# Performance work log

Hardware: AMD Instinct MI355X
Metric: run time of the kernel (lower is better)

The kernel has to match this reference:

```python
import jax, jax.numpy as jnp
import numpy as np


def setup_inputs() -> dict:
    key = jax.random.key(0)
    kx, kw = jax.random.split(key)
    A_MAX = 16  # activations in [0, 2**A_bits - 1] = [0, 15]
    W_MAX = 15  # torch.randint(0, 2**W_bits - 1) -> [0, 14]
    x = jax.random.randint(kx, (32, 256, 56, 56), 0, A_MAX, dtype=jnp.int32)
    weight = jax.random.randint(kw, (256, 256, 3, 3), 0, W_MAX, dtype=jnp.int32)
    return {"x": x, "weight": weight}


def reference(x, weight):
    # Low-bit quantized conv2d: direct_conv2d(x.int(), w.int(), stride=1) with the
    # module's crop for (k=3, padding=1) is equivalent to a conv with padding=1.
    # Max accumulator value = 15*14*9*256 < 2**24, so fp32 accumulation is exact.
    xf = x.astype(jnp.float32)
    wf = weight.astype(jnp.float32)
    y = jax.lax.conv_general_dilated(
        xf, wf,
        window_strides=(1, 1),
        padding=((1, 1), (1, 1)),
        dimension_numbers=("NCHW", "OIHW", "NCHW"),
    )
    return y.astype(jnp.int32)  # [32, 256, 56, 56]
```

## Files before the change

### kernel.cpp

```cpp
#include <hip/hip_runtime.h>

typedef int v4i  __attribute__((ext_vector_type(4)));
typedef int v16i __attribute__((ext_vector_type(16)));

#define N_IMG   32
#define C_IN    256
#define HWDIM   56
#define HW2     3136
#define OUT_TOT 25690112
#define OUT_NSTR 802816

#define PXB     272
#define PPI     3364
#define XP_IMG  915008
#define XP_SLACK 4096
#define WP_CB2STR 73728
#define WP_BYTES  589824ull

#define S_TILE  64
#define TILES_PER_IMG 49
#define WIN_B   50048

__global__ void dc_x_to_nhwc(const int* __restrict__ x, unsigned int* __restrict__ x8,
                             int n0) {
    __shared__ unsigned int lds[64 * 65];
    const int t = threadIdx.x;
    const int w = t & 63, q = t >> 6;
    const int nl = blockIdx.x / HWDIM, h = blockIdx.x % HWDIM;

    if (w < HWDIM) {
        const int* xb = x + (size_t)(n0 + nl) * OUT_NSTR + h * HWDIM + w;
        #pragma unroll
        for (int it = 0; it < 16; ++it) {
            const int cg4 = q * 16 + it;
            const int ci0 = cg4 * 4;
            unsigned v  =  ((unsigned)xb[(ci0 + 0) * HW2] & 0xff);
            v |= ((unsigned)xb[(ci0 + 1) * HW2] & 0xff) << 8;
            v |= ((unsigned)xb[(ci0 + 2) * HW2] & 0xff) << 16;
            v |= ((unsigned)xb[(ci0 + 3) * HW2] & 0xff) << 24;
            lds[w * 65 + cg4] = v;
        }
    }
    __syncthreads();
    unsigned int* ob = x8 + (size_t)nl * (PPI * (PXB / 4)) + ((h + 1) * 58 + 1) * (PXB / 4);
    #pragma unroll
    for (int it = 0; it < 14; ++it) {
        const int f = it * 256 + t;
        const int w2 = f >> 6, cg = f & 63;
        if (w2 < HWDIM) ob[w2 * (PXB / 4) + cg] = lds[w2 * 65 + cg];
    }
}

__global__ void dc_halo(unsigned int* __restrict__ x8) {
    const int nl = blockIdx.x;
    const int t = threadIdx.x;
    if (t < 228) {
        int h, w;
        if (t < 58)       { h = 0;        w = t; }
        else if (t < 116) { h = 57;       w = t - 58; }
        else if (t < 172) { h = t - 115;  w = 0; }
        else              { h = t - 171;  w = 57; }
        unsigned int* p = x8 + ((size_t)nl * PPI + h * 58 + w) * (PXB / 4);
        #pragma unroll
        for (int i = 0; i < PXB / 4; ++i) p[i] = 0;
    }
}

__global__ void dc_pack_w(const int* __restrict__ wt, unsigned int* __restrict__ wp) {
    const int tid = blockIdx.x * 256 + threadIdx.x;
    const int jq = tid & 3;
    const int l  = (tid >> 2) & 63;
    const int kb = (tid >> 8) & 7;
    const int r  = tid >> 11;
    const int t  = r % 9;
    const int cb2 = r / 9;
    const int co  = cb2 * 32 + (l & 31);
    const int ci0 = kb * 32 + (l >> 5) * 16 + jq * 4;
    const int kh = t / 3, kw = t - kh * 3;
    unsigned v = 0;
    #pragma unroll
    for (int k = 0; k < 4; ++k) {
        unsigned b = (unsigned)wt[((co * C_IN + ci0 + k) * 3 + kh) * 3 + kw];
        v |= (b & 0xff) << (8 * k);
    }
    wp[tid] = v;
}

__device__ __forceinline__ void gll16(const char* g, char* l) {
    __builtin_amdgcn_global_load_lds(
        (const __attribute__((address_space(1))) unsigned int*)g,
        (__attribute__((address_space(3))) unsigned int*)l, 16, 0, 0);
}

__global__ __launch_bounds__(256, 3) void dc_mfma(const char* __restrict__ x8,
                                                  const char* __restrict__ wp,
                                                  int* __restrict__ out, int nwg) {
    extern __shared__ __align__(16) char xs[];

    const int bid = blockIdx.x;
    const int q = nwg >> 3, r = nwg & 7;
    const int xcd = bid & 7, bidx = bid >> 3;
    const int wgid = (xcd < r ? xcd * (q + 1) : r * (q + 1) + (xcd - r) * q) + bidx;

    const int nl = wgid / TILES_PER_IMG, st = wgid - nl * TILES_PER_IMG;

    const int tid = threadIdx.x;
    const int l = tid & 63, wid = tid >> 6;
    const int lane31 = l & 31, hi = l >> 5;

    const int hw0 = st * S_TILE;
    const int h0 = hw0 / HWDIM, w0 = hw0 - h0 * HWDIM;
    const int p0 = h0 * 58 + w0;
    const char* gsrc = x8 + (size_t)nl * XP_IMG + (size_t)p0 * PXB;

    #pragma unroll
    for (int c = 0; c < 13; ++c) {
        const int off = (c * 256 + tid) * 16;
        if (off < WIN_B) gll16(gsrc + off, xs + off);
    }

    int breg[2], outb[2];
    #pragma unroll
    for (int ni = 0; ni < 2; ++ni) {
        const int hw = hw0 + ni * 32 + lane31;
        const int h = hw / HWDIM, w = hw - h * HWDIM;
        const int p = (h + 1) * 58 + (w + 1);
        breg[ni] = (p - p0) * PXB + hi * 16 - 16048;
        outb[ni] = nl * OUT_NSTR + hw;
    }

    const char* wb0 = wp + (wid * 2) * WP_CB2STR + l * 16;
    const char* wb1 = wb0 + WP_CB2STR;

    const int xoffp[9] = {
        16048 - 59 * PXB, 16048 - 58 * PXB, 16048 - 57 * PXB,
        16048 - 1 * PXB,  16048,            16048 + 1 * PXB,
        16048 + 57 * PXB, 16048 + 58 * PXB, 16048 + 59 * PXB
    };

    __syncthreads();

    v16i acc[2][2] = {};
    v4i wa[4][2];
    v4i xb[2][2];

    wa[0][0] = *(const v4i*)(wb0);
    wa[0][1] = *(const v4i*)(wb1);
    wa[1][0] = *(const v4i*)(wb0 + 1024);
    wa[1][1] = *(const v4i*)(wb1 + 1024);
    wa[2][0] = *(const v4i*)(wb0 + 2048);
    wa[2][1] = *(const v4i*)(wb1 + 2048);
    xb[0][0] = *(const v4i*)(xs + breg[0] + xoffp[0]);
    xb[0][1] = *(const v4i*)(xs + breg[1] + xoffp[0]);

    #pragma unroll
    for (int j = 0; j < 72; ++j) {
        const int jc = j & 3;
        const int pc = j & 1;
        if (j + 3 < 72) {
            const int jn = (j + 3) & 3;
            wa[jn][0] = *(const v4i*)(wb0 + (j + 3) * 1024);
            wa[jn][1] = *(const v4i*)(wb1 + (j + 3) * 1024);
        }
        if (j + 1 < 72) {
            const int t1 = (j + 1) >> 3, kb1 = (j + 1) & 7;
            const int xo = xoffp[t1] + kb1 * 32;
            xb[pc ^ 1][0] = *(const v4i*)(xs + breg[0] + xo);
            xb[pc ^ 1][1] = *(const v4i*)(xs + breg[1] + xo);
        }
        __builtin_amdgcn_s_setprio(1);
        acc[0][0] = __builtin_amdgcn_mfma_i32_32x32x32_i8(wa[jc][0], xb[pc][0], acc[0][0], 0, 0, 0);
        acc[0][1] = __builtin_amdgcn_mfma_i32_32x32x32_i8(wa[jc][0], xb[pc][1], acc[0][1], 0, 0, 0);
        acc[1][0] = __builtin_amdgcn_mfma_i32_32x32x32_i8(wa[jc][1], xb[pc][0], acc[1][0], 0, 0, 0);
        acc[1][1] = __builtin_amdgcn_mfma_i32_32x32x32_i8(wa[jc][1], xb[pc][1], acc[1][1], 0, 0, 0);
        __builtin_amdgcn_s_setprio(0);
    }

    #pragma unroll
    for (int mi = 0; mi < 2; ++mi) {
        #pragma unroll
        for (int ni = 0; ni < 2; ++ni) {
            const v16i c = acc[mi][ni];
            int* ob = out + outb[ni] + (wid * 64 + mi * 32 + 4 * hi) * HW2;
            #pragma unroll
            for (int rr = 0; rr < 16; ++rr) {
                __builtin_nontemporal_store(c[rr], ob + ((rr & 3) + 8 * (rr >> 2)) * HW2);
            }
        }
    }
}

__global__ void dc_naive(const int* __restrict__ x, const int* __restrict__ wt,
                         int* __restrict__ out) {
    const int idx = blockIdx.x * 256 + threadIdx.x;
    if (idx >= OUT_TOT) return;
    const int w = idx % HWDIM;
    const int h = (idx / HWDIM) % HWDIM;
    const int co = (idx / HW2) & 255;
    const int n = idx / OUT_NSTR;
    const int* xn = x + n * OUT_NSTR;
    const int* wo = wt + co * (C_IN * 9);
    int acc = 0;
    for (int ci = 0; ci < C_IN; ++ci) {
        const int* xc = xn + ci * HW2;
        const int* wc = wo + ci * 9;
        #pragma unroll
        for (int kh = 0; kh < 3; ++kh) {
            const int hh = h + kh - 1;
            if ((unsigned)hh >= HWDIM) continue;
            #pragma unroll
            for (int kw = 0; kw < 3; ++kw) {
                const int ww = w + kw - 1;
                if ((unsigned)ww >= HWDIM) continue;
                acc += xc[hh * HWDIM + ww] * wc[kh * 3 + kw];
            }
        }
    }
    out[idx] = acc;
}

extern "C" void kernel_launch(void* const* d_in, const int* in_sizes, int n_in,
                              void* d_out, int out_size, void* d_ws, size_t ws_size,
                              hipStream_t stream) {
    const int* x  = (const int*)d_in[0];
    const int* wt = (const int*)d_in[1];
    int* out = (int*)d_out;

    int chunk = 0;
    const int cand[4] = {32, 16, 8, 4};
    for (int i = 0; i < 4; ++i) {
        if ((size_t)cand[i] * XP_IMG + XP_SLACK + WP_BYTES <= ws_size) { chunk = cand[i]; break; }
    }

    if (chunk > 0) {
        char* x8 = (char*)d_ws;
        const size_t x8_bytes = (size_t)chunk * XP_IMG + XP_SLACK;
        unsigned int* wp = (unsigned int*)(x8 + x8_bytes);
        hipLaunchKernelGGL(dc_halo, dim3(chunk), dim3(256), 0, stream, (unsigned int*)x8);
        hipLaunchKernelGGL(dc_pack_w, dim3(576), dim3(256), 0, stream, wt, wp);
        for (int n0 = 0; n0 < N_IMG; n0 += chunk) {
            hipLaunchKernelGGL(dc_x_to_nhwc, dim3(chunk * HWDIM), dim3(256), 0, stream,
                               x, (unsigned int*)x8, n0);
            const int nwg = chunk * TILES_PER_IMG;
            hipLaunchKernelGGL(dc_mfma, dim3(nwg), dim3(256), WIN_B, stream,
                               (const char*)x8, (const char*)wp,
                               out + (size_t)n0 * OUT_NSTR, nwg);
        }
        return;
    }

    hipLaunchKernelGGL(dc_naive, dim3((OUT_TOT + 255) / 256), dim3(256), 0, stream,
                       x, wt, out);
}
```

Measured before the change: 92.98 us.

## Use 8x8 spatial tiles to shrink LDS halo window and raise occupancy

Replaces the linear 64-pixel row-strip tile with an 8x8 spatial tile. The kernel then loads a 10x10 padded halo window (27200 bytes) into LDS in place of the multi-row strip (50048 bytes). The smaller LDS footprint allows launch bounds of 4 workgroups per CU instead of 3, which should improve latency hiding and cut redundant halo loads. The trade-offs are a row-wise gather with per-thread div/mod address computation and tighter register limits that could cause spills.

```diff
diff --git a/kernel.cpp b/kernel.cpp
--- a/kernel.cpp
+++ b/kernel.cpp
@@ -17,9 +17,9 @@
 #define WP_CB2STR 73728
 #define WP_BYTES  589824ull
 
-#define S_TILE  64
 #define TILES_PER_IMG 49
-#define WIN_B   50048
+#define WIN_B   27200
+#define WROWB   15776
 
 __global__ void dc_x_to_nhwc(const int* __restrict__ x, unsigned int* __restrict__ x8,
                              int n0) {
@@ -92,7 +92,7 @@
         (__attribute__((address_space(3))) unsigned int*)l, 16, 0, 0);
 }
 
-__global__ __launch_bounds__(256, 3) void dc_mfma(const char* __restrict__ x8,
+__global__ __launch_bounds__(256, 4) void dc_mfma(const char* __restrict__ x8,
                                                   const char* __restrict__ wp,
                                                   int* __restrict__ out, int nwg) {
     extern __shared__ __align__(16) char xs[];
@@ -103,39 +103,40 @@
     const int wgid = (xcd < r ? xcd * (q + 1) : r * (q + 1) + (xcd - r) * q) + bidx;
 
     const int nl = wgid / TILES_PER_IMG, st = wgid - nl * TILES_PER_IMG;
+    const int th = st / 7, tw = st - th * 7;
+    const int h0 = th * 8, w0 = tw * 8;
 
     const int tid = threadIdx.x;
     const int l = tid & 63, wid = tid >> 6;
     const int lane31 = l & 31, hi = l >> 5;
-
-    const int hw0 = st * S_TILE;
-    const int h0 = hw0 / HWDIM, w0 = hw0 - h0 * HWDIM;
-    const int p0 = h0 * 58 + w0;
-    const char* gsrc = x8 + (size_t)nl * XP_IMG + (size_t)p0 * PXB;
-
-    #pragma unroll
-    for (int c = 0; c < 13; ++c) {
-        const int off = (c * 256 + tid) * 16;
-        if (off < WIN_B) gll16(gsrc + off, xs + off);
+    const int r4 = lane31 >> 3, c8 = lane31 & 7;
+
+    const char* gsrc = x8 + (size_t)nl * XP_IMG + (size_t)(h0 * 58 + w0) * PXB;
+
+    #pragma unroll
+    for (int c2 = 0; c2 < 7; ++c2) {
+        const int flat = c2 * 256 + tid;
+        if (flat < 1700) {
+            const int row = flat / 170, col = flat - row * 170;
+            gll16(gsrc + row * WROWB + col * 16, xs + flat * 16);
+        }
     }
 
     int breg[2], outb[2];
     #pragma unroll
     for (int ni = 0; ni < 2; ++ni) {
-        const int hw = hw0 + ni * 32 + lane31;
-        const int h = hw / HWDIM, w = hw - h * HWDIM;
-        const int p = (h + 1) * 58 + (w + 1);
-        breg[ni] = (p - p0) * PXB + hi * 16 - 16048;
-        outb[ni] = nl * OUT_NSTR + hw;
+        const int rr = r4 + ni * 4;
+        breg[ni] = ((rr + 1) * 10 + (c8 + 1)) * PXB + hi * 16;
+        outb[ni] = nl * OUT_NSTR + (h0 + rr) * HWDIM + (w0 + c8);
     }
 
     const char* wb0 = wp + (wid * 2) * WP_CB2STR + l * 16;
     const char* wb1 = wb0 + WP_CB2STR;
 
     const int xoffp[9] = {
-        16048 - 59 * PXB, 16048 - 58 * PXB, 16048 - 57 * PXB,
-        16048 - 1 * PXB,  16048,            16048 + 1 * PXB,
-        16048 + 57 * PXB, 16048 + 58 * PXB, 16048 + 59 * PXB
+        -11 * PXB, -10 * PXB, -9 * PXB,
+        -1 * PXB,   0,          1 * PXB,
+        9 * PXB,   10 * PXB,  11 * PXB
     };
 
     __syncthreads();
```

Result: slower. 178.2 us (+91.7%).

## Replace padded NHWC pixel stride with XOR-swizzled layout for LDS conflict avoidance

Applied to the files above, without the earlier changes.

Removes the 16-byte padding per pixel in the int8 NHWC buffer (272 to 256 bytes) and instead XOR-swizzles 16-byte channel chunks by pixel index, so LDS reads in the MFMA loop stay bank-conflict-free. This shrinks the global staging buffer and the LDS window, cutting load traffic and LDS footprint. The x fragment loads are no longer double-buffered a step ahead but issued right before each MFMA group, which could expose LDS latency; the address math per tap also grows.

```diff
diff --git a/kernel.cpp b/kernel.cpp
--- a/kernel.cpp
+++ b/kernel.cpp
@@ -10,16 +10,16 @@
 #define OUT_TOT 25690112
 #define OUT_NSTR 802816
 
-#define PXB     272
+#define PXB     256
 #define PPI     3364
-#define XP_IMG  915008
+#define XP_IMG  861184
 #define XP_SLACK 4096
 #define WP_CB2STR 73728
 #define WP_BYTES  589824ull
 
 #define S_TILE  64
 #define TILES_PER_IMG 49
-#define WIN_B   50048
+#define WIN_B   47104
 
 __global__ void dc_x_to_nhwc(const int* __restrict__ x, unsigned int* __restrict__ x8,
                              int n0) {
@@ -42,12 +42,16 @@
         }
     }
     __syncthreads();
-    unsigned int* ob = x8 + (size_t)nl * (PPI * (PXB / 4)) + ((h + 1) * 58 + 1) * (PXB / 4);
+    unsigned int* ob = x8 + (size_t)nl * (XP_IMG / 4) + ((h + 1) * 58 + 1) * (PXB / 4);
     #pragma unroll
     for (int it = 0; it < 14; ++it) {
         const int f = it * 256 + t;
         const int w2 = f >> 6, cg = f & 63;
-        if (w2 < HWDIM) ob[w2 * (PXB / 4) + cg] = lds[w2 * 65 + cg];
+        if (w2 < HWDIM) {
+            const int key = ((h + 1) * 58 + w2 + 1) & 15;
+            const int cg2 = (((cg >> 2) ^ key) << 2) | (cg & 3);
+            ob[w2 * (PXB / 4) + cg2] = lds[w2 * 65 + cg];
+        }
     }
 }
 
@@ -114,35 +118,30 @@
     const char* gsrc = x8 + (size_t)nl * XP_IMG + (size_t)p0 * PXB;
 
     #pragma unroll
-    for (int c = 0; c < 13; ++c) {
+    for (int c = 0; c < 12; ++c) {
         const int off = (c * 256 + tid) * 16;
         if (off < WIN_B) gll16(gsrc + off, xs + off);
     }
 
-    int breg[2], outb[2];
+    int rbase[2], Pb[2], outb[2];
     #pragma unroll
     for (int ni = 0; ni < 2; ++ni) {
         const int hw = hw0 + ni * 32 + lane31;
         const int h = hw / HWDIM, w = hw - h * HWDIM;
-        const int p = (h + 1) * 58 + (w + 1);
-        breg[ni] = (p - p0) * PXB + hi * 16 - 16048;
+        Pb[ni] = (h + 1) * 58 + (w + 1);
+        rbase[ni] = Pb[ni] - p0;
         outb[ni] = nl * OUT_NSTR + hw;
     }
 
     const char* wb0 = wp + (wid * 2) * WP_CB2STR + l * 16;
     const char* wb1 = wb0 + WP_CB2STR;
 
-    const int xoffp[9] = {
-        16048 - 59 * PXB, 16048 - 58 * PXB, 16048 - 57 * PXB,
-        16048 - 1 * PXB,  16048,            16048 + 1 * PXB,
-        16048 + 57 * PXB, 16048 + 58 * PXB, 16048 + 59 * PXB
-    };
+    const int dtap[9] = {-59, -58, -57, -1, 0, 1, 57, 58, 59};
 
     __syncthreads();
 
     v16i acc[2][2] = {};
     v4i wa[4][2];
-    v4i xb[2][2];
 
     wa[0][0] = *(const v4i*)(wb0);
     wa[0][1] = *(const v4i*)(wb1);
@@ -150,30 +149,35 @@
     wa[1][1] = *(const v4i*)(wb1 + 1024);
     wa[2][0] = *(const v4i*)(wb0 + 2048);
     wa[2][1] = *(const v4i*)(wb1 + 2048);
-    xb[0][0] = *(const v4i*)(xs + breg[0] + xoffp[0]);
-    xb[0][1] = *(const v4i*)(xs + breg[1] + xoffp[0]);
-
-    #pragma unroll
-    for (int j = 0; j < 72; ++j) {
-        const int jc = j & 3;
-        const int pc = j & 1;
-        if (j + 3 < 72) {
-            const int jn = (j + 3) & 3;
-            wa[jn][0] = *(const v4i*)(wb0 + (j + 3) * 1024);
-            wa[jn][1] = *(const v4i*)(wb1 + (j + 3) * 1024);
-        }
-        if (j + 1 < 72) {
-            const int t1 = (j + 1) >> 3, kb1 = (j + 1) & 7;
-            const int xo = xoffp[t1] + kb1 * 32;
-            xb[pc ^ 1][0] = *(const v4i*)(xs + breg[0] + xo);
-            xb[pc ^ 1][1] = *(const v4i*)(xs + breg[1] + xo);
-        }
-        __builtin_amdgcn_s_setprio(1);
-        acc[0][0] = __builtin_amdgcn_mfma_i32_32x32x32_i8(wa[jc][0], xb[pc][0], acc[0][0], 0, 0, 0);
-        acc[0][1] = __builtin_amdgcn_mfma_i32_32x32x32_i8(wa[jc][0], xb[pc][1], acc[0][1], 0, 0, 0);
-        acc[1][0] = __builtin_amdgcn_mfma_i32_32x32x32_i8(wa[jc][1], xb[pc][0], acc[1][0], 0, 0, 0);
-        acc[1][1] = __builtin_amdgcn_mfma_i32_32x32x32_i8(wa[jc][1], xb[pc][1], acc[1][1], 0, 0, 0);
-        __builtin_amdgcn_s_setprio(0);
+
+    #pragma unroll
+    for (int t = 0; t < 9; ++t) {
+        int xbase[2], xkey[2];
+        #pragma unroll
+        for (int ni = 0; ni < 2; ++ni) {
+            const int key = (Pb[ni] + dtap[t]) & 15;
+            xbase[ni] = (rbase[ni] + dtap[t]) * PXB + ((hi ^ (key & 1)) << 4);
+            xkey[ni] = (key >> 1) & 7;
+        }
+        #pragma unroll
+        for (int kb = 0; kb < 8; ++kb) {
+            const int j = t * 8 + kb;
+            const int jc = j & 3;
+            if (j + 3 < 72) {
+                const int jn = (j + 3) & 3;
+                wa[jn][0] = *(const v4i*)(wb0 + (j + 3) * 1024);
+                wa[jn][1] = *(const v4i*)(wb1 + (j + 3) * 1024);
+            }
+            const v4i xf0 = *(const v4i*)(xs + xbase[0] + ((kb ^ xkey[0]) << 5));
+            const v4i xf1 = *(const v4i*)(xs + xbase[1] + ((kb ^ xkey[1]) << 5));
+
+            __builtin_amdgcn_s_setprio(1);
+            acc[0][0] = __builtin_amdgcn_mfma_i32_32x32x32_i8(wa[jc][0], xf0, acc[0][0], 0, 0, 0);
+            acc[0][1] = __builtin_amdgcn_mfma_i32_32x32x32_i8(wa[jc][0], xf1, acc[0][1], 0, 0, 0);
+            acc[1][0] = __builtin_amdgcn_mfma_i32_32x32x32_i8(wa[jc][1], xf0, acc[1][0], 0, 0, 0);
+            acc[1][1] = __builtin_amdgcn_mfma_i32_32x32x32_i8(wa[jc][1], xf1, acc[1][1], 0, 0, 0);
+            __builtin_amdgcn_s_setprio(0);
+        }
     }
 
     #pragma unroll
```

New measurement: 96.87 us. +4.2%, slower.
